# Performance work log

Measured on AMD Instinct MI355X. Metric: run time of the kernel, lower is better.

## Reference

```python
import jax, jax.numpy as jnp
import numpy as np

N = 50000
E = 800000
C = 64
NEG_SLOPE = 0.2


def gat_conv(x, edge_index, W, att_src, att_dst, bias, heads, out_ch):
    """PyG GATConv forward (concat=True, add_self_loops=True).
    x: [N, in], edge_index: [2, E] (row0=src j, row1=dst i),
    W: [in, heads*out_ch], att_src/att_dst: [heads, out_ch], bias: [heads*out_ch].
    """
    n = x.shape[0]
    loop = jnp.arange(n, dtype=edge_index.dtype)
    src = jnp.concatenate([edge_index[0], loop])
    dst = jnp.concatenate([edge_index[1], loop])

    xl = (x @ W).reshape(n, heads, out_ch)            # [N, H, F]
    a_src = jnp.einsum('nhf,hf->nh', xl, att_src)      # [N, H]
    a_dst = jnp.einsum('nhf,hf->nh', xl, att_dst)      # [N, H]

    alpha = jax.nn.leaky_relu(a_src[src] + a_dst[dst], NEG_SLOPE)  # [E', H]
    # segment softmax over incoming edges of each destination node
    amax = jax.ops.segment_max(alpha, dst, num_segments=n)
    alpha = jnp.exp(alpha - amax[dst])
    denom = jax.ops.segment_sum(alpha, dst, num_segments=n)
    alpha = alpha / denom[dst]

    # gather source features, weight, scatter-add to destinations
    msg = xl[src] * alpha[:, :, None]                  # [E', H, F]
    out = jax.ops.segment_sum(msg, dst, num_segments=n)  # [N, H, F]
    return out.reshape(n, heads * out_ch) + bias


def setup_inputs() -> dict:
    key = jax.random.key(0)
    ks = jax.random.split(key, 12)
    x = jax.random.normal(ks[0], (N, C), dtype=jnp.float32)
    undirected = jax.random.randint(ks[1], (2, E), 0, N, dtype=jnp.int32)
    directed = jax.random.randint(ks[2], (2, E), 0, N, dtype=jnp.int32)

    s1 = 1.0 / np.sqrt(C)
    s2 = 1.0 / np.sqrt(2 * C)
    W1 = jax.random.normal(ks[3], (C, 2 * C), dtype=jnp.float32) * s1
    att_src1 = jax.random.normal(ks[4], (2, C), dtype=jnp.float32) * s1
    att_dst1 = jax.random.normal(ks[5], (2, C), dtype=jnp.float32) * s1
    b1 = jnp.zeros((2 * C,), dtype=jnp.float32)

    W2 = jax.random.normal(ks[6], (2 * C, 4 * C), dtype=jnp.float32) * s2
    att_src2 = jax.random.normal(ks[7], (2, 2 * C), dtype=jnp.float32) * s2
    att_dst2 = jax.random.normal(ks[8], (2, 2 * C), dtype=jnp.float32) * s2
    b2 = jnp.zeros((4 * C,), dtype=jnp.float32)

    return {
        'x': x,
        'undirected_edges_small': undirected,
        'directed_edges_small': directed,
        'W1': W1, 'att_src1': att_src1, 'att_dst1': att_dst1, 'b1': b1,
        'W2': W2, 'att_src2': att_src2, 'att_dst2': att_dst2, 'b2': b2,
    }


def reference(x, undirected_edges_small, directed_edges_small,
              W1, att_src1, att_dst1, b1,
              W2, att_src2, att_dst2, b2):
    h = gat_conv(x, undirected_edges_small, W1, att_src1, att_dst1, b1,
                 heads=2, out_ch=C)            # [N, 2C]
    out = gat_conv(h, directed_edges_small, W2, att_src2, att_dst2, b2,
                   heads=2, out_ch=2 * C)      # [N, 4C]
    return out
```

## Files before the change

kernel.cpp:

```cpp
#include <hip/hip_runtime.h>
#include <stdint.h>

#define N_NODES 50000
#define N_EDGES 800000
#define CAP 64
#define NBUCK 400
#define BSZ 125
#define BCAP 2816

typedef __attribute__((ext_vector_type(8))) short bf16x8;
typedef __attribute__((ext_vector_type(4))) float f32x4;

__device__ __forceinline__ float b2f_bits(unsigned int lo16) {
    union { unsigned int i; float f; } v; v.i = lo16 << 16; return v.f;
}
__device__ __forceinline__ unsigned short f2b(float f) {
    union { float f; unsigned int i; } v; v.f = f;
    unsigned int x = v.i;
    return (unsigned short)((x + 0x7fffu + ((x >> 16) & 1u)) >> 16);
}
__device__ __forceinline__ void split2(float v, unsigned short& h, unsigned short& l) {
    h = f2b(v);
    l = f2b(v - b2f_bits(h));
}
__device__ __forceinline__ void unpack8(const uint4 u, float* f) {
    f[0] = b2f_bits(u.x & 0xffffu); f[1] = b2f_bits(u.x >> 16);
    f[2] = b2f_bits(u.y & 0xffffu); f[3] = b2f_bits(u.y >> 16);
    f[4] = b2f_bits(u.z & 0xffffu); f[5] = b2f_bits(u.z >> 16);
    f[6] = b2f_bits(u.w & 0xffffu); f[7] = b2f_bits(u.w >> 16);
}

__global__ __launch_bounds__(256) void splitX_kernel(
    const float* __restrict__ X,
    unsigned short* __restrict__ Xh, unsigned short* __restrict__ Xl, int total4)
{
    const int i = blockIdx.x * 256 + threadIdx.x;
    if (i >= total4) return;
    const float4 v = ((const float4*)X)[i];
    ushort4 h, l;
    split2(v.x, h.x, l.x); split2(v.y, h.y, l.y);
    split2(v.z, h.z, l.z); split2(v.w, h.w, l.w);
    ((ushort4*)Xh)[i] = h;
    ((ushort4*)Xl)[i] = l;
}

__global__ __launch_bounds__(256) void splitWT_kernel(
    const float* __restrict__ W,
    unsigned short* __restrict__ WhT, unsigned short* __restrict__ WlT, int K, int N)
{
    const int i = blockIdx.x * 256 + threadIdx.x;
    if (i >= N * K) return;
    const int n = i / K, k = i % K;
    const float v = W[(size_t)k * N + n];
    unsigned short h, l;
    split2(v, h, l);
    WhT[i] = h; WlT[i] = l;
}

template<int K, int N, int CT>
__global__ __launch_bounds__(512) void mfma_gemm_kernel(
    const unsigned short* __restrict__ Xh,
    const unsigned short* __restrict__ Xl,
    const unsigned short* __restrict__ WhT,
    const unsigned short* __restrict__ WlT,
    unsigned short* __restrict__ XL, int M)
{
    constexpr int KC = K / 32;
    const int wave = threadIdx.x >> 6;
    const int lane = threadIdx.x & 63;
    const int lr = lane & 15;
    const int lk = (lane >> 4) * 8;
    const int c0 = wave * CT * 16;

    bf16x8 aw_h[CT][KC], aw_l[CT][KC];
#pragma unroll
    for (int t = 0; t < CT; ++t) {
        const unsigned short* wr  = WhT + (size_t)(c0 + t * 16 + lr) * K + lk;
        const unsigned short* wr2 = WlT + (size_t)(c0 + t * 16 + lr) * K + lk;
#pragma unroll
        for (int c = 0; c < KC; ++c) {
            aw_h[t][c] = *(const bf16x8*)(wr + c * 32);
            aw_l[t][c] = *(const bf16x8*)(wr2 + c * 32);
        }
    }

    auto loadB = [&](bf16x8 (&bh)[KC], bf16x8 (&bl)[KC], int sidx) {
        const unsigned short* xr  = Xh + (size_t)(sidx * 16 + lr) * K + lk;
        const unsigned short* xr2 = Xl + (size_t)(sidx * 16 + lr) * K + lk;
#pragma unroll
        for (int c = 0; c < KC; ++c) {
            bh[c] = *(const bf16x8*)(xr + c * 32);
            bl[c] = *(const bf16x8*)(xr2 + c * 32);
        }
    };
    auto compute = [&](bf16x8 (&bh)[KC], bf16x8 (&bl)[KC], int sidx) {
#pragma unroll
        for (int t = 0; t < CT; ++t) {
            f32x4 acc = {0.f, 0.f, 0.f, 0.f};
#pragma unroll
            for (int c = 0; c < KC; ++c)
                acc = __builtin_amdgcn_mfma_f32_16x16x32_bf16(aw_h[t][c], bh[c], acc, 0, 0, 0);
#pragma unroll
            for (int c = 0; c < KC; ++c)
                acc = __builtin_amdgcn_mfma_f32_16x16x32_bf16(aw_h[t][c], bl[c], acc, 0, 0, 0);
#pragma unroll
            for (int c = 0; c < KC; ++c)
                acc = __builtin_amdgcn_mfma_f32_16x16x32_bf16(aw_l[t][c], bh[c], acc, 0, 0, 0);
            ushort4 r;
            r.x = f2b(acc[0]); r.y = f2b(acc[1]); r.z = f2b(acc[2]); r.w = f2b(acc[3]);
            *(ushort4*)(XL + (size_t)(sidx * 16 + lr) * N + c0 + t * 16 + ((lane >> 4) << 2)) = r;
        }
    };

    const int NSTRIP = M / 16;
    const int nb = gridDim.x;
    int s = blockIdx.x;
    bf16x8 b0h[KC], b0l[KC], b1h[KC], b1l[KC];
    if (s < NSTRIP) loadB(b0h, b0l, s);
    while (s < NSTRIP) {
        const int sn = s + nb;
        if (sn < NSTRIP) loadB(b1h, b1l, sn);
        compute(b0h, b0l, s);
        if (sn >= NSTRIP) break;
        const int sn2 = sn + nb;
        if (sn2 < NSTRIP) loadB(b0h, b0l, sn2);
        compute(b1h, b1l, sn);
        s = sn2;
    }
}

template<int F>
__global__ __launch_bounds__(256) void att_kernel(
    const unsigned short* __restrict__ XL,
    const float* __restrict__ att_s,
    const float* __restrict__ att_d,
    float* __restrict__ a_src, float* __restrict__ a_dst, int n)
{
    constexpr int CPL = F / 64;
    const int node = (blockIdx.x * 256 + threadIdx.x) >> 6;
    const int lane = threadIdx.x & 63;
    if (node >= n) return;
    const unsigned short* row = XL + (size_t)node * F + lane * CPL;
    float v[CPL];
    if constexpr (CPL == 2) {
        const unsigned int u = *(const unsigned int*)row;
        v[0] = b2f_bits(u & 0xffffu); v[1] = b2f_bits(u >> 16);
    } else {
        const uint2 u = *(const uint2*)row;
        v[0] = b2f_bits(u.x & 0xffffu); v[1] = b2f_bits(u.x >> 16);
        v[2] = b2f_bits(u.y & 0xffffu); v[3] = b2f_bits(u.y >> 16);
    }
    float s1 = 0.f, s2 = 0.f;
#pragma unroll
    for (int i = 0; i < CPL; ++i) {
        s1 += v[i] * att_s[lane * CPL + i];
        s2 += v[i] * att_d[lane * CPL + i];
    }
#pragma unroll
    for (int o = 1; o < 32; o <<= 1) {
        s1 += __shfl_xor(s1, o);
        s2 += __shfl_xor(s2, o);
    }
    if ((lane & 31) == 0) {
        const int head = lane >> 5;
        a_src[node * 2 + head] = s1;
        a_dst[node * 2 + head] = s2;
    }
}

__global__ __launch_bounds__(256) void bucket_kernel(
    const int* __restrict__ e1, const int* __restrict__ e2, int ne,
    int* __restrict__ gcur, unsigned int* __restrict__ stage)
{
    const int layer = blockIdx.x & 1;
    const int bslot = blockIdx.x >> 1;
    const int nbl = gridDim.x >> 1;
    const int* __restrict__ eix = layer ? e2 : e1;
    int* cur = gcur + layer * NBUCK;
    unsigned int* __restrict__ stg = stage + (size_t)layer * NBUCK * BCAP;

    __shared__ int cnt_lds[NBUCK];
    __shared__ int base_lds[NBUCK];
    constexpr int EPT = 16;
    constexpr int CHUNK = 256 * EPT;

    for (int base = bslot * CHUNK; base < ne; base += nbl * CHUNK) {
        for (int i = threadIdx.x; i < NBUCK; i += 256) cnt_lds[i] = 0;
        __syncthreads();

        unsigned int rec[EPT];
        int bk[EPT];
#pragma unroll
        for (int i = 0; i < EPT; ++i) {
            const int e = base + i * 256 + threadIdx.x;
            bk[i] = -1;
            if (e < ne) {
                const int s = eix[e];
                const int d = eix[ne + e];
                if ((unsigned)d < (unsigned)N_NODES) {
                    const int b = d / BSZ;
                    bk[i] = b;
                    rec[i] = (unsigned)s | ((unsigned)(d - b * BSZ) << 16);
                    atomicAdd(&cnt_lds[b], 1);
                }
            }
        }
        __syncthreads();
        for (int i = threadIdx.x; i < NBUCK; i += 256) {
            const int c = cnt_lds[i];
            base_lds[i] = c ? atomicAdd(&cur[i], c) : 0;
            cnt_lds[i] = 0;
        }
        __syncthreads();
#pragma unroll
        for (int i = 0; i < EPT; ++i) {
            if (bk[i] >= 0) {
                const int idx = base_lds[bk[i]] + atomicAdd(&cnt_lds[bk[i]], 1);
                if (idx < BCAP) stg[(size_t)bk[i] * BCAP + idx] = rec[i];
            }
        }
        __syncthreads();
    }
}

__global__ __launch_bounds__(256) void place_kernel(
    const unsigned int* __restrict__ stage, const int* __restrict__ gcur,
    int* __restrict__ cnt1, int* __restrict__ cnt2,
    int* __restrict__ ss1, int* __restrict__ ss2)
{
    const int layer = blockIdx.x & 1;
    const int bucket = blockIdx.x >> 1;
    int m = gcur[layer * NBUCK + bucket];
    m = m < BCAP ? m : BCAP;
    const unsigned int* __restrict__ stg =
        stage + ((size_t)(layer * NBUCK + bucket)) * BCAP;
    int* __restrict__ cnt = layer ? cnt2 : cnt1;
    int* __restrict__ ss  = layer ? ss2 : ss1;
    const int d0 = bucket * BSZ;

    __shared__ int c_lds[BSZ];
    __shared__ __align__(16) unsigned int img[BSZ * CAP];

    for (int i = threadIdx.x; i < BSZ; i += 256) c_lds[i] = 0;
    __syncthreads();

    for (int i = threadIdx.x; i < m; i += 256) {
        const unsigned int v = stg[i];
        const int dr = (int)(v >> 16);
        const int slot = atomicAdd(&c_lds[dr], 1);
        if (slot < CAP) img[dr * CAP + slot] = v & 0xffffu;
    }
    __syncthreads();

    uint4* dst4 = (uint4*)(ss + (size_t)d0 * CAP);
    const uint4* src4 = (const uint4*)img;
    constexpr int NV4 = BSZ * CAP / 4;
    for (int i = threadIdx.x; i < NV4; i += 256) dst4[i] = src4[i];
    for (int i = threadIdx.x; i < BSZ; i += 256) {
        const int c = c_lds[i];
        cnt[d0 + i] = c < CAP ? c : CAP;
    }
}

template<int F, int EPI, bool SPLIT>
__global__ __launch_bounds__(256) void aggregate_kernel(
    const unsigned short* __restrict__ XL,
    const float* __restrict__ a_src, const float* __restrict__ a_dst,
    const int* __restrict__ cnt, const int* __restrict__ src_bins,
    const float* __restrict__ bias,
    float* __restrict__ OUT,
    unsigned short* __restrict__ OH, unsigned short* __restrict__ OL, int n)
{
    constexpr int SUBW = 64 / EPI;
    static_assert(F / SUBW == 8, "8 cols per lane");
    constexpr int NB = 8 / EPI;

    const int node = (blockIdx.x * 256 + threadIdx.x) >> 6;
    const int lane = threadIdx.x & 63;
    if (node >= n) return;
    const int halfLane = lane & (SUBW - 1);
    const int sub = lane / SUBW;
    const int head = (halfLane >= SUBW / 2) ? 1 : 0;

    const int s = node * CAP;
    int deg = cnt[node];
    deg = deg < CAP ? deg : CAP;
    const int e = s + deg;
    const float2 ad2 = *(const float2*)(a_dst + node * 2);
    const float ahead = head ? ad2.y : ad2.x;

    float acc[8];
#pragma unroll
    for (int k = 0; k < 8; ++k) acc[k] = 0.f;
    float den = 0.f;

    int p = s;
    for (; p + 8 <= e; p += 8) {
        int j[NB];
#pragma unroll
        for (int g = 0; g < NB; ++g) j[g] = src_bins[p + g * EPI + sub];
        float A[NB];
#pragma unroll
        for (int g = 0; g < NB; ++g) A[g] = a_src[j[g] * 2 + head];
        uint4 u[NB];
#pragma unroll
        for (int g = 0; g < NB; ++g)
            u[g] = *(const uint4*)(XL + (size_t)j[g] * F + halfLane * 8);
#pragma unroll
        for (int g = 0; g < NB; ++g) {
            float l = A[g] + ahead;
            l = (l > 0.f) ? l : 0.2f * l;
            const float w = __expf(l);
            den += w;
            float f[8];
            unpack8(u[g], f);
#pragma unroll
            for (int k = 0; k < 8; ++k) acc[k] += w * f[k];
        }
    }
    for (; p < e; p += EPI) {
        const int pos = p + sub;
        const int pc = (pos < e) ? pos : (e - 1);
        const int j = src_bins[pc];
        const float A = a_src[j * 2 + head];
        const uint4 u = *(const uint4*)(XL + (size_t)j * F + halfLane * 8);
        float l = A + ahead;
        l = (l > 0.f) ? l : 0.2f * l;
        const float w = (pos < e) ? __expf(l) : 0.f;
        den += w;
        float f[8];
        unpack8(u, f);
#pragma unroll
        for (int k = 0; k < 8; ++k) acc[k] += w * f[k];
    }

    if (sub == 0) {
        const float2 as2 = *(const float2*)(a_src + node * 2);
        float l = (head ? as2.y : as2.x) + ahead;
        l = (l > 0.f) ? l : 0.2f * l;
        const float w = __expf(l);
        den += w;
        const uint4 u = *(const uint4*)(XL + (size_t)node * F + halfLane * 8);
        float f[8];
        unpack8(u, f);
#pragma unroll
        for (int k = 0; k < 8; ++k) acc[k] += w * f[k];
    }

#pragma unroll
    for (int off = SUBW; off < 64; off <<= 1) {
        den += __shfl_xor(den, off);
#pragma unroll
        for (int k = 0; k < 8; ++k) acc[k] += __shfl_xor(acc[k], off);
    }

    if (sub == 0) {
        const float inv = 1.f / den;
        const float* b = bias + halfLane * 8;
        float vals[8];
#pragma unroll
        for (int k = 0; k < 8; ++k) vals[k] = acc[k] * inv + b[k];
        if constexpr (SPLIT) {
            ushort4 h0, h1, l0, l1;
            split2(vals[0], h0.x, l0.x); split2(vals[1], h0.y, l0.y);
            split2(vals[2], h0.z, l0.z); split2(vals[3], h0.w, l0.w);
            split2(vals[4], h1.x, l1.x); split2(vals[5], h1.y, l1.y);
            split2(vals[6], h1.z, l1.z); split2(vals[7], h1.w, l1.w);
            unsigned short* oh = OH + (size_t)node * F + halfLane * 8;
            unsigned short* ol = OL + (size_t)node * F + halfLane * 8;
            *(ushort4*)oh = h0; *(ushort4*)(oh + 4) = h1;
            *(ushort4*)ol = l0; *(ushort4*)(ol + 4) = l1;
        } else {
            float* o = OUT + (size_t)node * F + halfLane * 8;
            float4 r0, r1;
            r0.x = vals[0]; r0.y = vals[1]; r0.z = vals[2]; r0.w = vals[3];
            r1.x = vals[4]; r1.y = vals[5]; r1.z = vals[6]; r1.w = vals[7];
            *(float4*)o = r0;
            *(float4*)(o + 4) = r1;
        }
    }
}

extern "C" void kernel_launch(void* const* d_in, const int* in_sizes, int n_in,
                              void* d_out, int out_size, void* d_ws, size_t ws_size,
                              hipStream_t stream)
{
    const int N = N_NODES, E = N_EDGES;

    const float* x   = (const float*)d_in[0];
    const int*   und = (const int*)d_in[1];
    const int*   dir = (const int*)d_in[2];
    const float* W1  = (const float*)d_in[3];
    const float* as1 = (const float*)d_in[4];
    const float* ad1 = (const float*)d_in[5];
    const float* b1  = (const float*)d_in[6];
    const float* W2  = (const float*)d_in[7];
    const float* as2 = (const float*)d_in[8];
    const float* ad2 = (const float*)d_in[9];
    const float* b2  = (const float*)d_in[10];

    char* p = (char*)d_ws;
    auto alloc = [&](size_t bytes) {
        char* r = p;
        p += (bytes + 255) & ~(size_t)255;
        return r;
    };
    unsigned short* xl1 = (unsigned short*)alloc((size_t)N * 128 * 2);
    unsigned short* hh  = (unsigned short*)alloc((size_t)N * 128 * 2);
    unsigned short* hl  = (unsigned short*)alloc((size_t)N * 128 * 2);
    unsigned short* xl2 = (unsigned short*)alloc((size_t)N * 256 * 2);
    float* a_src   = (float*)alloc((size_t)N * 2 * 4);
    float* a_dst   = (float*)alloc((size_t)N * 2 * 4);
    int*   cnts    = (int*)alloc(((size_t)2 * N + 2 * NBUCK) * 4);
    int*   ss1     = (int*)alloc((size_t)N * CAP * 4);
    int*   ss2     = (int*)alloc((size_t)N * CAP * 4);
    unsigned short* w1ht = (unsigned short*)alloc((size_t)128 * 64 * 2);
    unsigned short* w1lt = (unsigned short*)alloc((size_t)128 * 64 * 2);
    unsigned short* w2ht = (unsigned short*)alloc((size_t)256 * 128 * 2);
    unsigned short* w2lt = (unsigned short*)alloc((size_t)256 * 128 * 2);
    int* cnt1 = cnts, * cnt2 = cnts + N, * gcur = cnts + 2 * N;

    unsigned int* stage = (unsigned int*)xl2;
    unsigned short* x1h = (unsigned short*)d_out;
    unsigned short* x1l = (unsigned short*)d_out + (size_t)N * 64;

    const int WB = (N * 64 + 255) / 256;

    hipMemsetAsync(gcur, 0, (size_t)2 * NBUCK * 4, stream);
    bucket_kernel<<<2 * 196, 256, 0, stream>>>(und, dir, E, gcur, stage);
    place_kernel<<<2 * NBUCK, 256, 0, stream>>>(stage, gcur, cnt1, cnt2, ss1, ss2);

    splitWT_kernel<<<(128 * 64 + 255) / 256, 256, 0, stream>>>(W1, w1ht, w1lt, 64, 128);
    splitWT_kernel<<<(256 * 128 + 255) / 256, 256, 0, stream>>>(W2, w2ht, w2lt, 128, 256);
    splitX_kernel<<<(N * 64 / 4 + 255) / 256, 256, 0, stream>>>(x, x1h, x1l, N * 64 / 4);

    mfma_gemm_kernel<64, 128, 1><<<768, 512, 0, stream>>>(x1h, x1l, w1ht, w1lt, xl1, N);
    att_kernel<128><<<WB, 256, 0, stream>>>(xl1, as1, ad1, a_src, a_dst, N);
    aggregate_kernel<128, 4, true><<<WB, 256, 0, stream>>>(
        xl1, a_src, a_dst, cnt1, ss1, b1, nullptr, hh, hl, N);

    mfma_gemm_kernel<128, 256, 2><<<384, 512, 0, stream>>>(hh, hl, w2ht, w2lt, xl2, N);
    att_kernel<256><<<WB, 256, 0, stream>>>(xl2, as2, ad2, a_src, a_dst, N);
    aggregate_kernel<256, 2, false><<<WB, 256, 0, stream>>>(
        xl2, a_src, a_dst, cnt2, ss2, b2, (float*)d_out, nullptr, nullptr, N);
}
```

Measured before the change: 308.3 us.

## Sort per-destination source lists by source group and unroll gather loop by 16

The place kernel now counts edges per (destination, source-group) pair, prefix-sums those counts, then places sources so each destination's list is grouped by the high bits of the source index. Neighbouring gathers in the aggregate loop then hit nearby rows of XL, which should improve cache locality. The aggregate kernel also gains a 16-edge unrolled main loop so more gathers are in flight at once. The cost is a second pass over staged edges with extra LDS atomics and higher register pressure in the aggregate kernel.

```diff
diff --git a/kernel.cpp b/kernel.cpp
--- a/kernel.cpp
+++ b/kernel.cpp
@@ -7,6 +7,8 @@
 #define NBUCK 400
 #define BSZ 125
 #define BCAP 2816
+#define NGRP 16
+#define GSHIFT 12
 
 typedef __attribute__((ext_vector_type(8))) short bf16x8;
 typedef __attribute__((ext_vector_type(4))) float f32x4;
@@ -238,16 +240,37 @@
     int* __restrict__ ss  = layer ? ss2 : ss1;
     const int d0 = bucket * BSZ;
 
-    __shared__ int c_lds[BSZ];
+    __shared__ int cg[BSZ * NGRP];
     __shared__ __align__(16) unsigned int img[BSZ * CAP];
 
-    for (int i = threadIdx.x; i < BSZ; i += 256) c_lds[i] = 0;
+    for (int i = threadIdx.x; i < BSZ * NGRP; i += 256) cg[i] = 0;
     __syncthreads();
 
     for (int i = threadIdx.x; i < m; i += 256) {
         const unsigned int v = stg[i];
         const int dr = (int)(v >> 16);
-        const int slot = atomicAdd(&c_lds[dr], 1);
+        const int g = (int)((v & 0xffffu) >> GSHIFT);
+        atomicAdd(&cg[dr * NGRP + g], 1);
+    }
+    __syncthreads();
+
+    if (threadIdx.x < BSZ) {
+        int run = 0;
+#pragma unroll
+        for (int g = 0; g < NGRP; ++g) {
+            const int c = cg[threadIdx.x * NGRP + g];
+            cg[threadIdx.x * NGRP + g] = run;
+            run += c;
+        }
+        cnt[d0 + threadIdx.x] = run < CAP ? run : CAP;
+    }
+    __syncthreads();
+
+    for (int i = threadIdx.x; i < m; i += 256) {
+        const unsigned int v = stg[i];
+        const int dr = (int)(v >> 16);
+        const int g = (int)((v & 0xffffu) >> GSHIFT);
+        const int slot = atomicAdd(&cg[dr * NGRP + g], 1);
         if (slot < CAP) img[dr * CAP + slot] = v & 0xffffu;
     }
     __syncthreads();
@@ -256,10 +279,6 @@
     const uint4* src4 = (const uint4*)img;
     constexpr int NV4 = BSZ * CAP / 4;
     for (int i = threadIdx.x; i < NV4; i += 256) dst4[i] = src4[i];
-    for (int i = threadIdx.x; i < BSZ; i += 256) {
-        const int c = c_lds[i];
-        cnt[d0 + i] = c < CAP ? c : CAP;
-    }
 }
 
 template<int F, int EPI, bool SPLIT>
@@ -274,6 +293,7 @@
     constexpr int SUBW = 64 / EPI;
     static_assert(F / SUBW == 8, "8 cols per lane");
     constexpr int NB = 8 / EPI;
+    constexpr int NB2 = 16 / EPI;
 
     const int node = (blockIdx.x * 256 + threadIdx.x) >> 6;
     const int lane = threadIdx.x & 63;
@@ -295,6 +315,29 @@
     float den = 0.f;
 
     int p = s;
+    for (; p + 16 <= e; p += 16) {
+        int j[NB2];
+#pragma unroll
+        for (int g = 0; g < NB2; ++g) j[g] = src_bins[p + g * EPI + sub];
+        float A[NB2];
+#pragma unroll
+        for (int g = 0; g < NB2; ++g) A[g] = a_src[j[g] * 2 + head];
+        uint4 u[NB2];
+#pragma unroll
+        for (int g = 0; g < NB2; ++g)
+            u[g] = *(const uint4*)(XL + (size_t)j[g] * F + halfLane * 8);
+#pragma unroll
+        for (int g = 0; g < NB2; ++g) {
+            float l = A[g] + ahead;
+            l = (l > 0.f) ? l : 0.2f * l;
+            const float w = __expf(l);
+            den += w;
+            float f[8];
+            unpack8(u[g], f);
+#pragma unroll
+            for (int k = 0; k < 8; ++k) acc[k] += w * f[k];
+        }
+    }
     for (; p + 8 <= e; p += 8) {
         int j[NB];
 #pragma unroll
```

Result: slower. 314.6 us (+2.0%).

## Aggregate before projecting and fold attention vectors into precomputed weight products

Applied to the files above, without the earlier changes.

The GAT layers are reordered so neighbor aggregation runs on the narrower input features (64 for layer 1, 128 for layer 2), per head, before the linear projection. The aggregated per-head results are then multiplied by W via MFMA GEMMs with bias fused in. Attention logits are computed directly from inputs using precomputed W·att products (and W1·W2·att plus a bias term for layer 2), so the separate attention passes over projected features go away. This cuts gather bandwidth in the edge-heavy aggregation. In exchange the intermediate buffers double per head, and layer 1 gathers only bf16-high inputs, which loses some precision.

```diff
diff --git a/kernel.cpp b/kernel.cpp
--- a/kernel.cpp
+++ b/kernel.cpp
@@ -23,25 +23,75 @@
     h = f2b(v);
     l = f2b(v - b2f_bits(h));
 }
-__device__ __forceinline__ void unpack8(const uint4 u, float* f) {
-    f[0] = b2f_bits(u.x & 0xffffu); f[1] = b2f_bits(u.x >> 16);
-    f[2] = b2f_bits(u.y & 0xffffu); f[3] = b2f_bits(u.y >> 16);
-    f[4] = b2f_bits(u.z & 0xffffu); f[5] = b2f_bits(u.z >> 16);
-    f[6] = b2f_bits(u.w & 0xffffu); f[7] = b2f_bits(u.w >> 16);
-}
-
-__global__ __launch_bounds__(256) void splitX_kernel(
-    const float* __restrict__ X,
-    unsigned short* __restrict__ Xh, unsigned short* __restrict__ Xl, int total4)
-{
-    const int i = blockIdx.x * 256 + threadIdx.x;
-    if (i >= total4) return;
-    const float4 v = ((const float4*)X)[i];
-    ushort4 h, l;
-    split2(v.x, h.x, l.x); split2(v.y, h.y, l.y);
-    split2(v.z, h.z, l.z); split2(v.w, h.w, l.w);
-    ((ushort4*)Xh)[i] = h;
-    ((ushort4*)Xl)[i] = l;
+
+__global__ __launch_bounds__(256) void proj_kernel(
+    const float* __restrict__ W1, const float* __restrict__ as1, const float* __restrict__ ad1,
+    const float* __restrict__ b1,
+    const float* __restrict__ W2, const float* __restrict__ as2, const float* __restrict__ ad2,
+    float* __restrict__ P1, float* __restrict__ q2, float* __restrict__ cs)
+{
+    __shared__ float p2[4 * 128];
+    for (int i = threadIdx.x; i < 4 * 128; i += 256) {
+        const int t = i >> 7, c = i & 127;
+        const int h = t & 1;
+        const float* att = (t < 2) ? as2 : ad2;
+        float s = 0.f;
+        for (int cc = 0; cc < 128; ++cc)
+            s += att[h * 128 + cc] * W2[(size_t)c * 256 + h * 128 + cc];
+        p2[i] = s;
+    }
+    {
+        const int t = threadIdx.x >> 6, k = threadIdx.x & 63;
+        const int h = t & 1;
+        const float* att = (t < 2) ? as1 : ad1;
+        float s = 0.f;
+        for (int c = 0; c < 64; ++c)
+            s += att[h * 64 + c] * W1[(size_t)k * 128 + h * 64 + c];
+        P1[t * 64 + k] = s;
+    }
+    __syncthreads();
+    for (int i = threadIdx.x; i < 4 * 128; i += 256) {
+        const int t = i >> 7, j = i & 127;
+        const int hc = j >> 6, k = j & 63;
+        float s = 0.f;
+        for (int c = 0; c < 64; ++c)
+            s += W1[(size_t)k * 128 + hc * 64 + c] * p2[t * 128 + hc * 64 + c];
+        q2[i] = s;
+    }
+    if (threadIdx.x < 4) {
+        const int t = threadIdx.x;
+        float s = 0.f;
+        for (int c = 0; c < 128; ++c) s += b1[c] * p2[t * 128 + c];
+        cs[t] = s;
+    }
+}
+
+__global__ __launch_bounds__(256) void prep1_kernel(
+    const float* __restrict__ X, const float* __restrict__ P1,
+    unsigned short* __restrict__ Xh,
+    float* __restrict__ a_src, float* __restrict__ a_dst, int n)
+{
+    const int node = (blockIdx.x * 256 + threadIdx.x) >> 4;
+    const int sl = threadIdx.x & 15;
+    if (node >= n) return;
+    const float4 v = *(const float4*)(X + (size_t)node * 64 + sl * 4);
+    ushort4 hv;
+    hv.x = f2b(v.x); hv.y = f2b(v.y); hv.z = f2b(v.z); hv.w = f2b(v.w);
+    *(ushort4*)(Xh + (size_t)node * 64 + sl * 4) = hv;
+    float d[4];
+#pragma unroll
+    for (int t = 0; t < 4; ++t) {
+        const float* pp = P1 + t * 64 + sl * 4;
+        d[t] = v.x * pp[0] + v.y * pp[1] + v.z * pp[2] + v.w * pp[3];
+    }
+#pragma unroll
+    for (int o = 1; o < 16; o <<= 1)
+#pragma unroll
+        for (int t = 0; t < 4; ++t) d[t] += __shfl_xor(d[t], o);
+    if (sl == 0) {
+        *(float2*)(a_src + node * 2) = make_float2(d[0], d[1]);
+        *(float2*)(a_dst + node * 2) = make_float2(d[2], d[3]);
+    }
 }
 
 __global__ __launch_bounds__(256) void splitWT_kernel(
@@ -55,117 +105,6 @@
     unsigned short h, l;
     split2(v, h, l);
     WhT[i] = h; WlT[i] = l;
-}
-
-template<int K, int N, int CT>
-__global__ __launch_bounds__(512) void mfma_gemm_kernel(
-    const unsigned short* __restrict__ Xh,
-    const unsigned short* __restrict__ Xl,
-    const unsigned short* __restrict__ WhT,
-    const unsigned short* __restrict__ WlT,
-    unsigned short* __restrict__ XL, int M)
-{
-    constexpr int KC = K / 32;
-    const int wave = threadIdx.x >> 6;
-    const int lane = threadIdx.x & 63;
-    const int lr = lane & 15;
-    const int lk = (lane >> 4) * 8;
-    const int c0 = wave * CT * 16;
-
-    bf16x8 aw_h[CT][KC], aw_l[CT][KC];
-#pragma unroll
-    for (int t = 0; t < CT; ++t) {
-        const unsigned short* wr  = WhT + (size_t)(c0 + t * 16 + lr) * K + lk;
-        const unsigned short* wr2 = WlT + (size_t)(c0 + t * 16 + lr) * K + lk;
-#pragma unroll
-        for (int c = 0; c < KC; ++c) {
-            aw_h[t][c] = *(const bf16x8*)(wr + c * 32);
-            aw_l[t][c] = *(const bf16x8*)(wr2 + c * 32);
-        }
-    }
-
-    auto loadB = [&](bf16x8 (&bh)[KC], bf16x8 (&bl)[KC], int sidx) {
-        const unsigned short* xr  = Xh + (size_t)(sidx * 16 + lr) * K + lk;
-        const unsigned short* xr2 = Xl + (size_t)(sidx * 16 + lr) * K + lk;
-#pragma unroll
-        for (int c = 0; c < KC; ++c) {
-            bh[c] = *(const bf16x8*)(xr + c * 32);
-            bl[c] = *(const bf16x8*)(xr2 + c * 32);
-        }
-    };
-    auto compute = [&](bf16x8 (&bh)[KC], bf16x8 (&bl)[KC], int sidx) {
-#pragma unroll
-        for (int t = 0; t < CT; ++t) {
-            f32x4 acc = {0.f, 0.f, 0.f, 0.f};
-#pragma unroll
-            for (int c = 0; c < KC; ++c)
-                acc = __builtin_amdgcn_mfma_f32_16x16x32_bf16(aw_h[t][c], bh[c], acc, 0, 0, 0);
-#pragma unroll
-            for (int c = 0; c < KC; ++c)
-                acc = __builtin_amdgcn_mfma_f32_16x16x32_bf16(aw_h[t][c], bl[c], acc, 0, 0, 0);
-#pragma unroll
-            for (int c = 0; c < KC; ++c)
-                acc = __builtin_amdgcn_mfma_f32_16x16x32_bf16(aw_l[t][c], bh[c], acc, 0, 0, 0);
-            ushort4 r;
-            r.x = f2b(acc[0]); r.y = f2b(acc[1]); r.z = f2b(acc[2]); r.w = f2b(acc[3]);
-            *(ushort4*)(XL + (size_t)(sidx * 16 + lr) * N + c0 + t * 16 + ((lane >> 4) << 2)) = r;
-        }
-    };
-
-    const int NSTRIP = M / 16;
-    const int nb = gridDim.x;
-    int s = blockIdx.x;
-    bf16x8 b0h[KC], b0l[KC], b1h[KC], b1l[KC];
-    if (s < NSTRIP) loadB(b0h, b0l, s);
-    while (s < NSTRIP) {
-        const int sn = s + nb;
-        if (sn < NSTRIP) loadB(b1h, b1l, sn);
-        compute(b0h, b0l, s);
-        if (sn >= NSTRIP) break;
-        const int sn2 = sn + nb;
-        if (sn2 < NSTRIP) loadB(b0h, b0l, sn2);
-        compute(b1h, b1l, sn);
-        s = sn2;
-    }
-}
-
-template<int F>
-__global__ __launch_bounds__(256) void att_kernel(
-    const unsigned short* __restrict__ XL,
-    const float* __restrict__ att_s,
-    const float* __restrict__ att_d,
-    float* __restrict__ a_src, float* __restrict__ a_dst, int n)
-{
-    constexpr int CPL = F / 64;
-    const int node = (blockIdx.x * 256 + threadIdx.x) >> 6;
-    const int lane = threadIdx.x & 63;
-    if (node >= n) return;
-    const unsigned short* row = XL + (size_t)node * F + lane * CPL;
-    float v[CPL];
-    if constexpr (CPL == 2) {
-        const unsigned int u = *(const unsigned int*)row;
-        v[0] = b2f_bits(u & 0xffffu); v[1] = b2f_bits(u >> 16);
-    } else {
-        const uint2 u = *(const uint2*)row;
-        v[0] = b2f_bits(u.x & 0xffffu); v[1] = b2f_bits(u.x >> 16);
-        v[2] = b2f_bits(u.y & 0xffffu); v[3] = b2f_bits(u.y >> 16);
-    }
-    float s1 = 0.f, s2 = 0.f;
-#pragma unroll
-    for (int i = 0; i < CPL; ++i) {
-        s1 += v[i] * att_s[lane * CPL + i];
-        s2 += v[i] * att_d[lane * CPL + i];
-    }
-#pragma unroll
-    for (int o = 1; o < 32; o <<= 1) {
-        s1 += __shfl_xor(s1, o);
-        s2 += __shfl_xor(s2, o);
-    }
-    if ((lane & 31) == 0) {
-        const int head = lane >> 5;
-        a_src[node * 2 + head] = s1;
-        a_dst[node * 2 + head] = s2;
-    }
 }
 
 __global__ __launch_bounds__(256) void bucket_kernel(
@@ -262,122 +201,391 @@
     }
 }
 
-template<int F, int EPI, bool SPLIT>
-__global__ __launch_bounds__(256) void aggregate_kernel(
-    const unsigned short* __restrict__ XL,
+__global__ __launch_bounds__(256) void agg1_kernel(
+    const unsigned short* __restrict__ XH, const float* __restrict__ X,
     const float* __restrict__ a_src, const float* __restrict__ a_dst,
-    const int* __restrict__ cnt, const int* __restrict__ src_bins,
-    const float* __restrict__ bias,
-    float* __restrict__ OUT,
-    unsigned short* __restrict__ OH, unsigned short* __restrict__ OL, int n)
-{
-    constexpr int SUBW = 64 / EPI;
-    static_assert(F / SUBW == 8, "8 cols per lane");
-    constexpr int NB = 8 / EPI;
-
+    const int* __restrict__ cnt, const int* __restrict__ bins,
+    unsigned short* __restrict__ AH, unsigned short* __restrict__ AL, int n)
+{
     const int node = (blockIdx.x * 256 + threadIdx.x) >> 6;
     const int lane = threadIdx.x & 63;
     if (node >= n) return;
-    const int halfLane = lane & (SUBW - 1);
-    const int sub = lane / SUBW;
-    const int head = (halfLane >= SUBW / 2) ? 1 : 0;
+    const int hl = lane & 15;
+    const int sub = lane >> 4;
 
     const int s = node * CAP;
-    int deg = cnt[node];
-    deg = deg < CAP ? deg : CAP;
+    int deg = cnt[node]; deg = deg < CAP ? deg : CAP;
     const int e = s + deg;
-    const float2 ad2 = *(const float2*)(a_dst + node * 2);
-    const float ahead = head ? ad2.y : ad2.x;
-
-    float acc[8];
-#pragma unroll
-    for (int k = 0; k < 8; ++k) acc[k] = 0.f;
-    float den = 0.f;
+    const float2 ad = *(const float2*)(a_dst + node * 2);
+
+    float acc0[4] = {0.f, 0.f, 0.f, 0.f}, acc1[4] = {0.f, 0.f, 0.f, 0.f};
+    float den0 = 0.f, den1 = 0.f;
 
     int p = s;
     for (; p + 8 <= e; p += 8) {
-        int j[NB];
-#pragma unroll
-        for (int g = 0; g < NB; ++g) j[g] = src_bins[p + g * EPI + sub];
-        float A[NB];
-#pragma unroll
-        for (int g = 0; g < NB; ++g) A[g] = a_src[j[g] * 2 + head];
-        uint4 u[NB];
-#pragma unroll
-        for (int g = 0; g < NB; ++g)
-            u[g] = *(const uint4*)(XL + (size_t)j[g] * F + halfLane * 8);
-#pragma unroll
-        for (int g = 0; g < NB; ++g) {
-            float l = A[g] + ahead;
-            l = (l > 0.f) ? l : 0.2f * l;
-            const float w = __expf(l);
-            den += w;
-            float f[8];
-            unpack8(u[g], f);
-#pragma unroll
-            for (int k = 0; k < 8; ++k) acc[k] += w * f[k];
-        }
-    }
-    for (; p < e; p += EPI) {
+        int j[2];
+        j[0] = bins[p + sub];
+        j[1] = bins[p + 4 + sub];
+        float2 A[2];
+        A[0] = *(const float2*)(a_src + j[0] * 2);
+        A[1] = *(const float2*)(a_src + j[1] * 2);
+        uint2 u[2];
+        u[0] = *(const uint2*)(XH + (size_t)j[0] * 64 + hl * 4);
+        u[1] = *(const uint2*)(XH + (size_t)j[1] * 64 + hl * 4);
+#pragma unroll
+        for (int g = 0; g < 2; ++g) {
+            float l0 = A[g].x + ad.x; l0 = l0 > 0.f ? l0 : 0.2f * l0;
+            float l1 = A[g].y + ad.y; l1 = l1 > 0.f ? l1 : 0.2f * l1;
+            const float w0 = __expf(l0), w1 = __expf(l1);
+            den0 += w0; den1 += w1;
+            float f[4];
+            f[0] = b2f_bits(u[g].x & 0xffffu); f[1] = b2f_bits(u[g].x >> 16);
+            f[2] = b2f_bits(u[g].y & 0xffffu); f[3] = b2f_bits(u[g].y >> 16);
+#pragma unroll
+            for (int k = 0; k < 4; ++k) { acc0[k] += w0 * f[k]; acc1[k] += w1 * f[k]; }
+        }
+    }
+    for (; p < e; p += 4) {
         const int pos = p + sub;
-        const int pc = (pos < e) ? pos : (e - 1);
-        const int j = src_bins[pc];
-        const float A = a_src[j * 2 + head];
-        const uint4 u = *(const uint4*)(XL + (size_t)j * F + halfLane * 8);
-        float l = A + ahead;
-        l = (l > 0.f) ? l : 0.2f * l;
-        const float w = (pos < e) ? __expf(l) : 0.f;
-        den += w;
-        float f[8];
-        unpack8(u, f);
-#pragma unroll
-        for (int k = 0; k < 8; ++k) acc[k] += w * f[k];
-    }
-
+        const int pc = pos < e ? pos : e - 1;
+        const int j = bins[pc];
+        const float2 A = *(const float2*)(a_src + j * 2);
+        const uint2 u = *(const uint2*)(XH + (size_t)j * 64 + hl * 4);
+        float l0 = A.x + ad.x; l0 = l0 > 0.f ? l0 : 0.2f * l0;
+        float l1 = A.y + ad.y; l1 = l1 > 0.f ? l1 : 0.2f * l1;
+        float w0 = __expf(l0), w1 = __expf(l1);
+        if (pos >= e) { w0 = 0.f; w1 = 0.f; }
+        den0 += w0; den1 += w1;
+        float f[4];
+        f[0] = b2f_bits(u.x & 0xffffu); f[1] = b2f_bits(u.x >> 16);
+        f[2] = b2f_bits(u.y & 0xffffu); f[3] = b2f_bits(u.y >> 16);
+#pragma unroll
+        for (int k = 0; k < 4; ++k) { acc0[k] += w0 * f[k]; acc1[k] += w1 * f[k]; }
+    }
     if (sub == 0) {
-        const float2 as2 = *(const float2*)(a_src + node * 2);
-        float l = (head ? as2.y : as2.x) + ahead;
-        l = (l > 0.f) ? l : 0.2f * l;
-        const float w = __expf(l);
-        den += w;
-        const uint4 u = *(const uint4*)(XL + (size_t)node * F + halfLane * 8);
-        float f[8];
-        unpack8(u, f);
-#pragma unroll
-        for (int k = 0; k < 8; ++k) acc[k] += w * f[k];
-    }
-
-#pragma unroll
-    for (int off = SUBW; off < 64; off <<= 1) {
-        den += __shfl_xor(den, off);
-#pragma unroll
-        for (int k = 0; k < 8; ++k) acc[k] += __shfl_xor(acc[k], off);
-    }
-
+        const float2 A = *(const float2*)(a_src + node * 2);
+        const float4 v = *(const float4*)(X + (size_t)node * 64 + hl * 4);
+        float l0 = A.x + ad.x; l0 = l0 > 0.f ? l0 : 0.2f * l0;
+        float l1 = A.y + ad.y; l1 = l1 > 0.f ? l1 : 0.2f * l1;
+        const float w0 = __expf(l0), w1 = __expf(l1);
+        den0 += w0; den1 += w1;
+        acc0[0] += w0 * v.x; acc0[1] += w0 * v.y; acc0[2] += w0 * v.z; acc0[3] += w0 * v.w;
+        acc1[0] += w1 * v.x; acc1[1] += w1 * v.y; acc1[2] += w1 * v.z; acc1[3] += w1 * v.w;
+    }
+#pragma unroll
+    for (int o = 16; o < 64; o <<= 1) {
+        den0 += __shfl_xor(den0, o); den1 += __shfl_xor(den1, o);
+#pragma unroll
+        for (int k = 0; k < 4; ++k) {
+            acc0[k] += __shfl_xor(acc0[k], o);
+            acc1[k] += __shfl_xor(acc1[k], o);
+        }
+    }
+    if (lane < 32) {
+        const int head = lane >> 4;
+        float vv[4];
+        if (head) {
+            const float inv = 1.f / den1;
+            vv[0] = acc1[0] * inv; vv[1] = acc1[1] * inv;
+            vv[2] = acc1[2] * inv; vv[3] = acc1[3] * inv;
+        } else {
+            const float inv = 1.f / den0;
+            vv[0] = acc0[0] * inv; vv[1] = acc0[1] * inv;
+            vv[2] = acc0[2] * inv; vv[3] = acc0[3] * inv;
+        }
+        ushort4 hv, lv;
+        split2(vv[0], hv.x, lv.x); split2(vv[1], hv.y, lv.y);
+        split2(vv[2], hv.z, lv.z); split2(vv[3], hv.w, lv.w);
+        const size_t off = (size_t)head * N_NODES * 64 + (size_t)node * 64 + hl * 4;
+        *(ushort4*)(AH + off) = hv;
+        *(ushort4*)(AL + off) = lv;
+    }
+}
+
+__global__ __launch_bounds__(256) void att2_kernel(
+    const unsigned short* __restrict__ A1H, const unsigned short* __restrict__ A1L,
+    const float* __restrict__ q2, const float* __restrict__ cs,
+    float* __restrict__ a_src, float* __restrict__ a_dst, int n)
+{
+    const int node = (blockIdx.x * 256 + threadIdx.x) >> 6;
+    const int lane = threadIdx.x & 63;
+    if (node >= n) return;
+    const int hc = lane >> 5;
+    const int k2 = (lane & 31) * 2;
+    const size_t off = (size_t)hc * N_NODES * 64 + (size_t)node * 64 + k2;
+    const unsigned int uh = *(const unsigned int*)(A1H + off);
+    const unsigned int ul = *(const unsigned int*)(A1L + off);
+    const float v0 = b2f_bits(uh & 0xffffu) + b2f_bits(ul & 0xffffu);
+    const float v1 = b2f_bits(uh >> 16) + b2f_bits(ul >> 16);
+    const int j = hc * 64 + k2;
+    float d[4];
+#pragma unroll
+    for (int t = 0; t < 4; ++t)
+        d[t] = v0 * q2[t * 128 + j] + v1 * q2[t * 128 + j + 1];
+#pragma unroll
+    for (int o = 1; o < 64; o <<= 1)
+#pragma unroll
+        for (int t = 0; t < 4; ++t) d[t] += __shfl_xor(d[t], o);
+    if (lane == 0) {
+        *(float2*)(a_src + node * 2) = make_float2(d[0] + cs[0], d[1] + cs[1]);
+        *(float2*)(a_dst + node * 2) = make_float2(d[2] + cs[2], d[3] + cs[3]);
+    }
+}
+
+__global__ __launch_bounds__(256) void agg2_kernel(
+    const unsigned short* __restrict__ HH, const unsigned short* __restrict__ HL,
+    const float* __restrict__ a_src, const float* __restrict__ a_dst,
+    const int* __restrict__ cnt, const int* __restrict__ bins,
+    unsigned short* __restrict__ AH, unsigned short* __restrict__ AL, int n)
+{
+    const int node = (blockIdx.x * 256 + threadIdx.x) >> 6;
+    const int lane = threadIdx.x & 63;
+    if (node >= n) return;
+    const int hl = lane & 31;
+    const int sub = lane >> 5;
+
+    const int s = node * CAP;
+    int deg = cnt[node]; deg = deg < CAP ? deg : CAP;
+    const int e = s + deg;
+    const float2 ad = *(const float2*)(a_dst + node * 2);
+
+    float acc0[4] = {0.f, 0.f, 0.f, 0.f}, acc1[4] = {0.f, 0.f, 0.f, 0.f};
+    float den0 = 0.f, den1 = 0.f;
+
+    int p = s;
+    for (; p + 8 <= e; p += 8) {
+        int j[4];
+#pragma unroll
+        for (int g = 0; g < 4; ++g) j[g] = bins[p + g * 2 + sub];
+        float2 A[4];
+#pragma unroll
+        for (int g = 0; g < 4; ++g) A[g] = *(const float2*)(a_src + j[g] * 2);
+        uint2 u[4];
+#pragma unroll
+        for (int g = 0; g < 4; ++g)
+            u[g] = *(const uint2*)(HH + (size_t)j[g] * 128 + hl * 4);
+#pragma unroll
+        for (int g = 0; g < 4; ++g) {
+            float l0 = A[g].x + ad.x; l0 = l0 > 0.f ? l0 : 0.2f * l0;
+            float l1 = A[g].y + ad.y; l1 = l1 > 0.f ? l1 : 0.2f * l1;
+            const float w0 = __expf(l0), w1 = __expf(l1);
+            den0 += w0; den1 += w1;
+            float f[4];
+            f[0] = b2f_bits(u[g].x & 0xffffu); f[1] = b2f_bits(u[g].x >> 16);
+            f[2] = b2f_bits(u[g].y & 0xffffu); f[3] = b2f_bits(u[g].y >> 16);
+#pragma unroll
+            for (int k = 0; k < 4; ++k) { acc0[k] += w0 * f[k]; acc1[k] += w1 * f[k]; }
+        }
+    }
+    for (; p < e; p += 2) {
+        const int pos = p + sub;
+        const int pc = pos < e ? pos : e - 1;
+        const int j = bins[pc];
+        const float2 A = *(const float2*)(a_src + j * 2);
+        const uint2 u = *(const uint2*)(HH + (size_t)j * 128 + hl * 4);
+        float l0 = A.x + ad.x; l0 = l0 > 0.f ? l0 : 0.2f * l0;
+        float l1 = A.y + ad.y; l1 = l1 > 0.f ? l1 : 0.2f * l1;
+        float w0 = __expf(l0), w1 = __expf(l1);
+        if (pos >= e) { w0 = 0.f; w1 = 0.f; }
+        den0 += w0; den1 += w1;
+        float f[4];
+        f[0] = b2f_bits(u.x & 0xffffu); f[1] = b2f_bits(u.x >> 16);
+        f[2] = b2f_bits(u.y & 0xffffu); f[3] = b2f_bits(u.y >> 16);
+#pragma unroll
+        for (int k = 0; k < 4; ++k) { acc0[k] += w0 * f[k]; acc1[k] += w1 * f[k]; }
+    }
     if (sub == 0) {
-        const float inv = 1.f / den;
-        const float* b = bias + halfLane * 8;
-        float vals[8];
-#pragma unroll
-        for (int k = 0; k < 8; ++k) vals[k] = acc[k] * inv + b[k];
-        if constexpr (SPLIT) {
-            ushort4 h0, h1, l0, l1;
-            split2(vals[0], h0.x, l0.x); split2(vals[1], h0.y, l0.y);
-            split2(vals[2], h0.z, l0.z); split2(vals[3], h0.w, l0.w);
-            split2(vals[4], h1.x, l1.x); split2(vals[5], h1.y, l1.y);
-            split2(vals[6], h1.z, l1.z); split2(vals[7], h1.w, l1.w);
-            unsigned short* oh = OH + (size_t)node * F + halfLane * 8;
-            unsigned short* ol = OL + (size_t)node * F + halfLane * 8;
-            *(ushort4*)oh = h0; *(ushort4*)(oh + 4) = h1;
-            *(ushort4*)ol = l0; *(ushort4*)(ol + 4) = l1;
+        const float2 A = *(const float2*)(a_src + node * 2);
+        const uint2 uh = *(const uint2*)(HH + (size_t)node * 128 + hl * 4);
+        const uint2 ul = *(const uint2*)(HL + (size_t)node * 128 + hl * 4);
+        float l0 = A.x + ad.x; l0 = l0 > 0.f ? l0 : 0.2f * l0;
+        float l1 = A.y + ad.y; l1 = l1 > 0.f ? l1 : 0.2f * l1;
+        const float w0 = __expf(l0), w1 = __expf(l1);
+        den0 += w0; den1 += w1;
+        float f[4];
+        f[0] = b2f_bits(uh.x & 0xffffu) + b2f_bits(ul.x & 0xffffu);
+        f[1] = b2f_bits(uh.x >> 16) + b2f_bits(ul.x >> 16);
+        f[2] = b2f_bits(uh.y & 0xffffu) + b2f_bits(ul.y & 0xffffu);
+        f[3] = b2f_bits(uh.y >> 16) + b2f_bits(ul.y >> 16);
+#pragma unroll
+        for (int k = 0; k < 4; ++k) { acc0[k] += w0 * f[k]; acc1[k] += w1 * f[k]; }
+    }
+    den0 += __shfl_xor(den0, 32); den1 += __shfl_xor(den1, 32);
+#pragma unroll
+    for (int k = 0; k < 4; ++k) {
+        acc0[k] += __shfl_xor(acc0[k], 32);
+        acc1[k] += __shfl_xor(acc1[k], 32);
+    }
+    {
+        const int head = sub;
+        float vv[4];
+        if (head) {
+            const float inv = 1.f / den1;
+            vv[0] = acc1[0] * inv; vv[1] = acc1[1] * inv;
+            vv[2] = acc1[2] * inv; vv[3] = acc1[3] * inv;
         } else {
-            float* o = OUT + (size_t)node * F + halfLane * 8;
-            float4 r0, r1;
-            r0.x = vals[0]; r0.y = vals[1]; r0.z = vals[2]; r0.w = vals[3];
-            r1.x = vals[4]; r1.y = vals[5]; r1.z = vals[6]; r1.w = vals[7];
-            *(float4*)o = r0;
-            *(float4*)(o + 4) = r1;
-        }
+            const float inv = 1.f / den0;
+            vv[0] = acc0[0] * inv; vv[1] = acc0[1] * inv;
+            vv[2] = acc0[2] * inv; vv[3] = acc0[3] * inv;
+        }
+        ushort4 hv, lv;
+        split2(vv[0], hv.x, lv.x); split2(vv[1], hv.y, lv.y);
+        split2(vv[2], hv.z, lv.z); split2(vv[3], hv.w, lv.w);
+        const size_t off = (size_t)head * N_NODES * 128 + (size_t)node * 128 + hl * 4;
+        *(ushort4*)(AH + off) = hv;
+        *(ushort4*)(AL + off) = lv;
+    }
+}
+
+__global__ __launch_bounds__(512) void gemm_h_kernel(
+    const unsigned short* __restrict__ AH, const unsigned short* __restrict__ AL,
+    const unsigned short* __restrict__ WTh, const unsigned short* __restrict__ WTl,
+    const float* __restrict__ b1,
+    unsigned short* __restrict__ HH, unsigned short* __restrict__ HL, int M)
+{
+    constexpr int K = 64, KC = 2;
+    const int wave = threadIdx.x >> 6;
+    const int lane = threadIdx.x & 63;
+    const int head = wave >> 2;
+    const int c0 = (wave & 3) * 16;
+    const int lr = lane & 15;
+    const int lk = (lane >> 4) * 8;
+    const int colg = head * 64 + c0 + ((lane >> 4) << 2);
+
+    bf16x8 awh[KC], awl[KC];
+    {
+        const unsigned short* wr  = WTh + (size_t)(head * 64 + c0 + lr) * K + lk;
+        const unsigned short* wr2 = WTl + (size_t)(head * 64 + c0 + lr) * K + lk;
+#pragma unroll
+        for (int c = 0; c < KC; ++c) {
+            awh[c] = *(const bf16x8*)(wr + c * 32);
+            awl[c] = *(const bf16x8*)(wr2 + c * 32);
+        }
+    }
+    const float4 bias = *(const float4*)(b1 + colg);
+    const unsigned short* XhB = AH + (size_t)head * M * 64;
+    const unsigned short* XlB = AL + (size_t)head * M * 64;
+
+    auto loadB = [&](bf16x8 (&bh)[KC], bf16x8 (&bl)[KC], int sidx) {
+        const unsigned short* xr  = XhB + (size_t)(sidx * 16 + lr) * 64 + lk;
+        const unsigned short* xr2 = XlB + (size_t)(sidx * 16 + lr) * 64 + lk;
+#pragma unroll
+        for (int c = 0; c < KC; ++c) {
+            bh[c] = *(const bf16x8*)(xr + c * 32);
+            bl[c] = *(const bf16x8*)(xr2 + c * 32);
+        }
+    };
+    auto compute = [&](bf16x8 (&bh)[KC], bf16x8 (&bl)[KC], int sidx) {
+        f32x4 acc = {0.f, 0.f, 0.f, 0.f};
+#pragma unroll
+        for (int c = 0; c < KC; ++c)
+            acc = __builtin_amdgcn_mfma_f32_16x16x32_bf16(awh[c], bh[c], acc, 0, 0, 0);
+#pragma unroll
+        for (int c = 0; c < KC; ++c)
+            acc = __builtin_amdgcn_mfma_f32_16x16x32_bf16(awh[c], bl[c], acc, 0, 0, 0);
+#pragma unroll
+        for (int c = 0; c < KC; ++c)
+            acc = __builtin_amdgcn_mfma_f32_16x16x32_bf16(awl[c], bh[c], acc, 0, 0, 0);
+        ushort4 hv, lv;
+        split2(acc[0] + bias.x, hv.x, lv.x); split2(acc[1] + bias.y, hv.y, lv.y);
+        split2(acc[2] + bias.z, hv.z, lv.z); split2(acc[3] + bias.w, hv.w, lv.w);
+        const size_t o = (size_t)(sidx * 16 + lr) * 128 + colg;
+        *(ushort4*)(HH + o) = hv;
+        *(ushort4*)(HL + o) = lv;
+    };
+
+    const int NSTRIP = M / 16;
+    const int nb = gridDim.x;
+    int s = blockIdx.x;
+    bf16x8 b0h[KC], b0l[KC], b1h_[KC], b1l_[KC];
+    if (s < NSTRIP) loadB(b0h, b0l, s);
+    while (s < NSTRIP) {
+        const int sn = s + nb;
+        if (sn < NSTRIP) loadB(b1h_, b1l_, sn);
+        compute(b0h, b0l, s);
+        if (sn >= NSTRIP) break;
+        const int sn2 = sn + nb;
+        if (sn2 < NSTRIP) loadB(b0h, b0l, sn2);
+        compute(b1h_, b1l_, sn);
+        s = sn2;
+    }
+}
+
+__global__ __launch_bounds__(512) void gemm_out_kernel(
+    const unsigned short* __restrict__ AH, const unsigned short* __restrict__ AL,
+    const unsigned short* __restrict__ WTh, const unsigned short* __restrict__ WTl,
+    const float* __restrict__ b2,
+    float* __restrict__ OUT, int M)
+{
+    constexpr int K = 128, KC = 4, CT = 2;
+    const int wave = threadIdx.x >> 6;
+    const int lane = threadIdx.x & 63;
+    const int head = wave >> 2;
+    const int c0 = (wave & 3) * 32;
+    const int lr = lane & 15;
+    const int lk = (lane >> 4) * 8;
+
+    bf16x8 awh[CT][KC], awl[CT][KC];
+    float4 bias[CT];
+    int colg[CT];
+#pragma unroll
+    for (int t = 0; t < CT; ++t) {
+        const unsigned short* wr  = WTh + (size_t)(head * 128 + c0 + t * 16 + lr) * K + lk;
+        const unsigned short* wr2 = WTl + (size_t)(head * 128 + c0 + t * 16 + lr) * K + lk;
+#pragma unroll
+        for (int c = 0; c < KC; ++c) {
+            awh[t][c] = *(const bf16x8*)(wr + c * 32);
+            awl[t][c] = *(const bf16x8*)(wr2 + c * 32);
+        }
+        colg[t] = head * 128 + c0 + t * 16 + ((lane >> 4) << 2);
+        bias[t] = *(const float4*)(b2 + colg[t]);
+    }
+    const unsigned short* XhB = AH + (size_t)head * M * 128;
+    const unsigned short* XlB = AL + (size_t)head * M * 128;
+
+    auto loadB = [&](bf16x8 (&bh)[KC], bf16x8 (&bl)[KC], int sidx) {
+        const unsigned short* xr  = XhB + (size_t)(sidx * 16 + lr) * 128 + lk;
+        const unsigned short* xr2 = XlB + (size_t)(sidx * 16 + lr) * 128 + lk;
+#pragma unroll
+        for (int c = 0; c < KC; ++c) {
+            bh[c] = *(const bf16x8*)(xr + c * 32);
+            bl[c] = *(const bf16x8*)(xr2 + c * 32);
+        }
+    };
+    auto compute = [&](bf16x8 (&bh)[KC], bf16x8 (&bl)[KC], int sidx) {
+#pragma unroll
+        for (int t = 0; t < CT; ++t) {
+            f32x4 acc = {0.f, 0.f, 0.f, 0.f};
+#pragma unroll
+            for (int c = 0; c < KC; ++c)
+                acc = __builtin_amdgcn_mfma_f32_16x16x32_bf16(awh[t][c], bh[c], acc, 0, 0, 0);
+#pragma unroll
+            for (int c = 0; c < KC; ++c)
+                acc = __builtin_amdgcn_mfma_f32_16x16x32_bf16(awh[t][c], bl[c], acc, 0, 0, 0);
+#pragma unroll
+            for (int c = 0; c < KC; ++c)
+                acc = __builtin_amdgcn_mfma_f32_16x16x32_bf16(awl[t][c], bh[c], acc, 0, 0, 0);
+            float4 o;
+            o.x = acc[0] + bias[t].x; o.y = acc[1] + bias[t].y;
+            o.z = acc[2] + bias[t].z; o.w = acc[3] + bias[t].w;
+            *(float4*)(OUT + (size_t)(sidx * 16 + lr) * 256 + colg[t]) = o;
+        }
+    };
+
+    const int NSTRIP = M / 16;
+    const int nb = gridDim.x;
+    int s = blockIdx.x;
+    bf16x8 b0h[KC], b0l[KC], b1h_[KC], b1l_[KC];
+    if (s < NSTRIP) loadB(b0h, b0l, s);
+    while (s < NSTRIP) {
+        const int sn = s + nb;
+        if (sn < NSTRIP) loadB(b1h_, b1l_, sn);
+        compute(b0h, b0l, s);
+        if (sn >= NSTRIP) break;
+        const int sn2 = sn + nb;
+        if (sn2 < NSTRIP) loadB(b0h, b0l, sn2);
+        compute(b1h_, b1l_, sn);
+        s = sn2;
     }
 }
 
@@ -405,42 +613,45 @@
         p += (bytes + 255) & ~(size_t)255;
         return r;
     };
-    unsigned short* xl1 = (unsigned short*)alloc((size_t)N * 128 * 2);
-    unsigned short* hh  = (unsigned short*)alloc((size_t)N * 128 * 2);
-    unsigned short* hl  = (unsigned short*)alloc((size_t)N * 128 * 2);
-    unsigned short* xl2 = (unsigned short*)alloc((size_t)N * 256 * 2);
-    float* a_src   = (float*)alloc((size_t)N * 2 * 4);
-    float* a_dst   = (float*)alloc((size_t)N * 2 * 4);
-    int*   cnts    = (int*)alloc(((size_t)2 * N + 2 * NBUCK) * 4);
-    int*   ss1     = (int*)alloc((size_t)N * CAP * 4);
-    int*   ss2     = (int*)alloc((size_t)N * CAP * 4);
-    unsigned short* w1ht = (unsigned short*)alloc((size_t)128 * 64 * 2);
-    unsigned short* w1lt = (unsigned short*)alloc((size_t)128 * 64 * 2);
-    unsigned short* w2ht = (unsigned short*)alloc((size_t)256 * 128 * 2);
-    unsigned short* w2lt = (unsigned short*)alloc((size_t)256 * 128 * 2);
+    unsigned short* agg2h = (unsigned short*)alloc((size_t)2 * N * 128 * 2);
+    unsigned short* agg2l = (unsigned short*)alloc((size_t)2 * N * 128 * 2);
+    unsigned short* hlbuf = (unsigned short*)alloc((size_t)N * 128 * 2);
+    int*   ss1   = (int*)alloc((size_t)N * CAP * 4);
+    int*   ss2   = (int*)alloc((size_t)N * CAP * 4);
+    float* a_src1 = (float*)alloc((size_t)N * 2 * 4);
+    float* a_dst1 = (float*)alloc((size_t)N * 2 * 4);
+    float* a_src2 = (float*)alloc((size_t)N * 2 * 4);
+    float* a_dst2 = (float*)alloc((size_t)N * 2 * 4);
+    int*   cnts  = (int*)alloc(((size_t)2 * N + 2 * NBUCK) * 4);
+    unsigned short* w1th = (unsigned short*)alloc((size_t)128 * 64 * 2);
+    unsigned short* w1tl = (unsigned short*)alloc((size_t)128 * 64 * 2);
+    unsigned short* w2th = (unsigned short*)alloc((size_t)256 * 128 * 2);
+    unsigned short* w2tl = (unsigned short*)alloc((size_t)256 * 128 * 2);
+    float* P1d = (float*)alloc(4 * 64 * 4);
+    float* q2d = (float*)alloc(4 * 128 * 4);
+    float* csd = (float*)alloc(4 * 4);
     int* cnt1 = cnts, * cnt2 = cnts + N, * gcur = cnts + 2 * N;
 
-    unsigned int* stage = (unsigned int*)xl2;
-    unsigned short* x1h = (unsigned short*)d_out;
-    unsigned short* x1l = (unsigned short*)d_out + (size_t)N * 64;
-
-    const int WB = (N * 64 + 255) / 256;
-
+    unsigned int* stage = (unsigned int*)agg2h;
+    unsigned short* hhbuf = (unsigned short*)ss1;
+    unsigned short* x1h   = (unsigned short*)d_out;
+    unsigned short* agg1h = (unsigned short*)d_out + (size_t)N * 64;
+    unsigned short* agg1l = (unsigned short*)d_out + (size_t)N * 64 + (size_t)N * 128;
+
+    const int WB = (N * 64) / 256;
+
+    proj_kernel<<<1, 256, 0, stream>>>(W1, as1, ad1, b1, W2, as2, ad2, P1d, q2d, csd);
     hipMemsetAsync(gcur, 0, (size_t)2 * NBUCK * 4, stream);
     bucket_kernel<<<2 * 196, 256, 0, stream>>>(und, dir, E, gcur, stage);
     place_kernel<<<2 * NBUCK, 256, 0, stream>>>(stage, gcur, cnt1, cnt2, ss1, ss2);
-
-    splitWT_kernel<<<(128 * 64 + 255) / 256, 256, 0, stream>>>(W1, w1ht, w1lt, 64, 128);
-    splitWT_kernel<<<(256 * 128 + 255) / 256, 256, 0, stream>>>(W2, w2ht, w2lt, 128, 256);
-    splitX_kernel<<<(N * 64 / 4 + 255) / 256, 256, 0, stream>>>(x, x1h, x1l, N * 64 / 4);
-
-    mfma_gemm_kernel<64, 128, 1><<<768, 512, 0, stream>>>(x1h, x1l, w1ht, w1lt, xl1, N);
-    att_kernel<128><<<WB, 256, 0, stream>>>(xl1, as1, ad1, a_src, a_dst, N);
-    aggregate_kernel<128, 4, true><<<WB, 256, 0, stream>>>(
-        xl1, a_src, a_dst, cnt1, ss1, b1, nullptr, hh, hl, N);
-
-    mfma_gemm_kernel<128, 256, 2><<<384, 512, 0, stream>>>(hh, hl, w2ht, w2lt, xl2, N);
-    att_kernel<256><<<WB, 256, 0, stream>>>(xl2, as2, ad2, a_src, a_dst, N);
-    aggregate_kernel<256, 2, false><<<WB, 256, 0, stream>>>(
-        xl2, a_src, a_dst, cnt2, ss2, b2, (float*)d_out, nullptr, nullptr, N);
-}
+    prep1_kernel<<<(N * 16) / 256, 256, 0, stream>>>(x, P1d, x1h, a_src1, a_dst1, N);
+    splitWT_kernel<<<(128 * 64 + 255) / 256, 256, 0, stream>>>(W1, w1th, w1tl, 64, 128);
+    splitWT_kernel<<<(256 * 128 + 255) / 256, 256, 0, stream>>>(W2, w2th, w2tl, 128, 256);
+
+    agg1_kernel<<<WB, 256, 0, stream>>>(x1h, x, a_src1, a_dst1, cnt1, ss1, agg1h, agg1l, N);
+    gemm_h_kernel<<<768, 512, 0, stream>>>(agg1h, agg1l, w1th, w1tl, b1, hhbuf, hlbuf, N);
+    att2_kernel<<<WB, 256, 0, stream>>>(agg1h, agg1l, q2d, csd, a_src2, a_dst2, N);
+
+    agg2_kernel<<<WB, 256, 0, stream>>>(hhbuf, hlbuf, a_src2, a_dst2, cnt2, ss2, agg2h, agg2l, N);
+    gemm_out_kernel<<<512, 512, 0, stream>>>(agg2h, agg2l, w2th, w2tl, b2, (float*)d_out, N);
+}
```

After: 297.1 us. 1.04x faster.
